# Kernel optimization log

Measured on AMD Instinct MI355X. Metric: run time of the kernel, lower is better.

## Reference

```python
import jax, jax.numpy as jnp
import numpy as np

B, L, D, V, d, N, H = 16, 1024, 50, 129, 64, 2, 8
DK = d // H           # 8
DFF = 2 * d           # 128
CVE = int(np.sqrt(d)) # 8
EPS = 1e-07 ** 2      # module squares epsilon
MASK_ATTN = -1e-30    # Transformer mask_value (as in source)
MASK_POOL = -1e+30    # Attention-pooling mask_value


def setup_inputs() -> dict:
    key = jax.random.key(0)
    ks = jax.random.split(key, 32)
    g = lambda i, shape, s=0.02: (jax.random.normal(ks[i], shape, dtype=jnp.float32) * s)
    inp = {
        'demo':   jax.random.normal(ks[0], (B, D), dtype=jnp.float32),
        'times':  jax.random.uniform(ks[1], (B, L), dtype=jnp.float32),
        'values': jax.random.normal(ks[2], (B, L), dtype=jnp.float32),
        'varis':  jax.random.randint(ks[3], (B, L), 0, V + 1),
        # variable embedding table
        'emb': g(4, (V + 1, d), 0.05),
        # CVE for values: Linear(1,CVE)+tanh+Linear(CVE,d,no bias)
        'vW1': g(5, (1, CVE), 0.5), 'vb1': jnp.zeros((CVE,), jnp.float32), 'vW2': g(6, (CVE, d), 0.1),
        # CVE for times
        'tW1': g(7, (1, CVE), 0.5), 'tb1': jnp.zeros((CVE,), jnp.float32), 'tW2': g(8, (CVE, d), 0.1),
        # Transformer params
        'Wq': g(9,  (N, H, d, DK), 0.1), 'Wk': g(10, (N, H, d, DK), 0.1),
        'Wv': g(11, (N, H, d, DK), 0.1), 'Wo': g(12, (N, H * DK, d), 0.1),
        'W1': g(13, (N, d, DFF), 0.1), 'b1': jnp.zeros((N, DFF), jnp.float32),
        'W2': g(14, (N, DFF, d), 0.1), 'b2': jnp.zeros((N, d), jnp.float32),
        'gamma': jnp.ones((2 * N,), jnp.float32), 'beta': jnp.zeros((2 * N,), jnp.float32),
        # Attention pooling: Linear(d,2d)+tanh+Linear(2d,1,no bias)
        'aW1': g(15, (d, 2 * d), 0.1), 'ab1': jnp.zeros((2 * d,), jnp.float32), 'aW2': g(16, (2 * d, 1), 0.1),
        # demo stack: Linear(D,2d)+tanh+Linear(2d,d)+tanh
        'dW1': g(17, (D, 2 * d), 0.1), 'db1': jnp.zeros((2 * d,), jnp.float32),
        'dW2': g(18, (2 * d, d), 0.1), 'db2': jnp.zeros((d,), jnp.float32),
        # output head: Linear(2d,1)+sigmoid+flatten
        'Wout': g(19, (2 * d, 1), 0.1), 'bout': jnp.zeros((1,), jnp.float32),
    }
    return inp


def _ln(X, g, b):
    mean = jnp.mean(X, axis=-1, keepdims=True)
    var = jnp.mean(jnp.square(X - mean), axis=-1, keepdims=True)
    return (X - mean) / jnp.sqrt(var + EPS) * g + b


def _forward(demo, times, values, varis, emb, vW1, vb1, vW2, tW1, tb1, tW2,
             Wq, Wk, Wv, Wo, W1, b1, W2, b2, gamma, beta,
             aW1, ab1, aW2, dW1, db1, dW2, db2, Wout, bout):
    mask = (varis > 0).astype(jnp.float32)  # [B,L]
    demo_enc = jnp.tanh(jnp.tanh(demo @ dW1 + db1) @ dW2 + db2)  # [B,d]
    varis_emb = emb[varis]                                       # [B,L,d]
    values_emb = jnp.tanh(values[..., None] @ vW1 + vb1) @ vW2   # [B,L,d]
    times_emb = jnp.tanh(times[..., None] @ tW1 + tb1) @ tW2     # [B,L,d]
    X = varis_emb + values_emb + times_emb

    mb = mask[:, None, None, :]  # [B,1,1,L] broadcasts over heads & query rows
    for i in range(N):
        q = jnp.einsum('bld,hdk->bhlk', X, Wq[i])
        k = jnp.einsum('bld,hdk->bhlk', X, Wk[i])
        v = jnp.einsum('bld,hdk->bhlk', X, Wv[i])
        A = jnp.einsum('bhlk,bhmk->bhlm', q, k)      # no 1/sqrt(dk) scaling (faithful)
        A = mb * A + (1.0 - mb) * MASK_ATTN
        A = jax.nn.softmax(A, axis=-1)
        O = jnp.einsum('bhlm,bhmk->bhlk', A, v)      # [B,H,L,DK]
        conc = jnp.transpose(O, (0, 2, 1, 3)).reshape(O.shape[0], O.shape[2], H * DK)
        X = X + conc @ Wo[i]
        X = _ln(X, gamma[2 * i], beta[2 * i])
        ffn = jax.nn.relu(X @ W1[i] + b1[i]) @ W2[i] + b2[i]
        X = X + ffn
        X = _ln(X, gamma[2 * i + 1], beta[2 * i + 1])

    aw = jnp.tanh(X @ aW1 + ab1) @ aW2               # [B,L,1]
    m = mask[..., None]
    aw = jax.nn.softmax(m * aw + (1.0 - m) * MASK_POOL, axis=-2)
    fused = jnp.sum(X * aw, axis=-2)                 # [B,d]
    conc = jnp.concatenate([fused, demo_enc], axis=-1)
    return jax.nn.sigmoid(conc @ Wout + bout).reshape(-1)  # [B]


def reference(demo, times, values, varis, emb, vW1, vb1, vW2, tW1, tb1, tW2,
              Wq, Wk, Wv, Wo, W1, b1, W2, b2, gamma, beta,
              aW1, ab1, aW2, dW1, db1, dW2, db2, Wout, bout):
    return _forward(demo, times, values, varis, emb, vW1, vb1, vW2, tW1, tb1, tW2,
                    Wq, Wk, Wv, Wo, W1, b1, W2, b2, gamma, beta,
                    aW1, ab1, aW2, dW1, db1, dW2, db2, Wout, bout)
```

## Files before the change

### kernel.cpp

```cpp
#include <hip/hip_runtime.h>
#include <math.h>


typedef __bf16 bf16x8 __attribute__((ext_vector_type(8)));
typedef __bf16 bf16x2 __attribute__((ext_vector_type(2)));
typedef float f32x16 __attribute__((ext_vector_type(16)));
typedef unsigned int uint4e __attribute__((ext_vector_type(4)));
typedef unsigned long long u64;

static __device__ __forceinline__ float wave_sum64(float x) {
#pragma unroll
    for (int off = 32; off > 0; off >>= 1) x += __shfl_xor(x, off, 64);
    return x;
}

static __device__ __forceinline__ unsigned pack2(float a, float b) {
    bf16x2 t; t[0] = (__bf16)a; t[1] = (__bf16)b;
    return __builtin_bit_cast(unsigned, t);
}

static __device__ __forceinline__ float exp2fast(float x) {
#if defined(__has_builtin) && __has_builtin(__builtin_amdgcn_exp2f)
    return __builtin_amdgcn_exp2f(x);
#else
    return exp2f(x);
#endif
}

static __device__ __forceinline__ void plswap(unsigned v, unsigned& lo, unsigned& hi_) {
#if defined(__has_builtin) && __has_builtin(__builtin_amdgcn_permlane32_swap)
    auto r = __builtin_amdgcn_permlane32_swap(v, v, false, false);
    lo = r[0]; hi_ = r[1];
#else
    unsigned x = __shfl_xor(v, 32, 64);
    bool h = (threadIdx.x & 32) != 0;
    lo = h ? x : v;
    hi_ = h ? v : x;
#endif
}

__global__ __launch_bounds__(256) void embed_kernel(
    const float* __restrict__ times, const float* __restrict__ values,
    const int* __restrict__ varis, const float* __restrict__ emb,
    const float* __restrict__ vW1, const float* __restrict__ vb1, const float* __restrict__ vW2,
    const float* __restrict__ tW1, const float* __restrict__ tb1, const float* __restrict__ tW2,
    float* __restrict__ X, float* __restrict__ mask)
{
    int row = blockIdx.x * 4 + (threadIdx.x >> 6);
    int c   = threadIdx.x & 63;
    float v = values[row];
    float t = times[row];
    int var = varis[row];
    if (c == 0) mask[row] = (var > 0) ? 1.0f : 0.0f;
    float th = 0.f;
    if (c < 8)       th = tanhf(fmaf(v, vW1[c], vb1[c]));
    else if (c < 16) th = tanhf(fmaf(t, tW1[c - 8], tb1[c - 8]));
    float acc = emb[var * 64 + c];
#pragma unroll
    for (int j = 0; j < 8; ++j) {
        acc = fmaf(__shfl(th, j, 64),     vW2[j * 64 + c], acc);
        acc = fmaf(__shfl(th, j + 8, 64), tW2[j * 64 + c], acc);
    }
    X[row * 64 + c] = acc;
}

__global__ __launch_bounds__(128) void demo_kernel(
    const float* __restrict__ demo, const float* __restrict__ dW1, const float* __restrict__ db1,
    const float* __restrict__ dW2, const float* __restrict__ db2, float* __restrict__ denc)
{
    __shared__ float sh[128];
    int b = blockIdx.x;
    int t = threadIdx.x;
    float a = db1[t];
    for (int j = 0; j < 50; ++j) a = fmaf(demo[b * 50 + j], dW1[j * 128 + t], a);
    sh[t] = tanhf(a);
    __syncthreads();
    if (t < 64) {
        float a2 = db2[t];
#pragma unroll 8
        for (int j = 0; j < 128; ++j) a2 = fmaf(sh[j], dW2[j * 64 + t], a2);
        denc[b * 64 + t] = tanhf(a2);
    }
}

__global__ __launch_bounds__(256) void qkv_kernel(
    const float* __restrict__ X, const float* __restrict__ mask,
    const float* __restrict__ Wq, const float* __restrict__ Wk, const float* __restrict__ Wv,
    __bf16* __restrict__ qbf, __bf16* __restrict__ kbf, __bf16* __restrict__ vtb)
{
    __shared__ __align__(16) unsigned char qsm[52224];
    float* sWq = (float*)qsm;
    float* sWk = sWq + 4352;
    float* sWv = sWk + 4352;
    int tid = threadIdx.x;
    for (int idx = tid; idx < 4096; idx += 256) {
        int h = idx >> 9, c = (idx >> 3) & 63, kk = idx & 7;
        int o = h * 8 + kk;
        sWq[o * 68 + c] = Wq[idx];
        sWk[o * 68 + c] = Wk[idx];
        sWv[o * 68 + c] = Wv[idx];
    }
    int row0 = blockIdx.x * 16;
    __syncthreads();
    int lane = tid & 63;
    int wv4 = (tid >> 6) * 4;
    float aq[4] = {0.f, 0.f, 0.f, 0.f};
    float ak[4] = {0.f, 0.f, 0.f, 0.f};
    float av[4] = {0.f, 0.f, 0.f, 0.f};
#pragma unroll
    for (int c = 0; c < 64; c += 4) {
        float4 xv[4];
#pragma unroll
        for (int rr = 0; rr < 4; ++rr)
            xv[rr] = *(const float4*)(X + (row0 + wv4 + rr) * 64 + c);
        float4 wq = *(const float4*)(sWq + lane * 68 + c);
        float4 wk = *(const float4*)(sWk + lane * 68 + c);
        float4 wvv= *(const float4*)(sWv + lane * 68 + c);
#pragma unroll
        for (int rr = 0; rr < 4; ++rr) {
            aq[rr] = fmaf(xv[rr].x, wq.x, aq[rr]);  aq[rr] = fmaf(xv[rr].y, wq.y, aq[rr]);
            aq[rr] = fmaf(xv[rr].z, wq.z, aq[rr]);  aq[rr] = fmaf(xv[rr].w, wq.w, aq[rr]);
            ak[rr] = fmaf(xv[rr].x, wk.x, ak[rr]);  ak[rr] = fmaf(xv[rr].y, wk.y, ak[rr]);
            ak[rr] = fmaf(xv[rr].z, wk.z, ak[rr]);  ak[rr] = fmaf(xv[rr].w, wk.w, ak[rr]);
            av[rr] = fmaf(xv[rr].x, wvv.x, av[rr]); av[rr] = fmaf(xv[rr].y, wvv.y, av[rr]);
            av[rr] = fmaf(xv[rr].z, wvv.z, av[rr]); av[rr] = fmaf(xv[rr].w, wvv.w, av[rr]);
        }
    }
    float aqr[4], akr[4], avr[4];
#pragma unroll
    for (int rr = 0; rr < 4; ++rr) {
        float km = mask[row0 + wv4 + rr];
        aqr[rr] = aq[rr] * 1.4426950408889634f;
        akr[rr] = (km != 0.f) ? ak[rr] : 0.f;
        avr[rr] = av[rr];
    }
    __syncthreads();
    __bf16* sQb = (__bf16*)qsm;
    __bf16* sKb = (__bf16*)(qsm + 2304);
    __bf16* sVt = (__bf16*)(qsm + 4608);
    int h = lane >> 3, kk = lane & 7;
#pragma unroll
    for (int rr = 0; rr < 4; ++rr) {
        int r = wv4 + rr;
        sQb[h * 136 + r * 8 + kk] = (__bf16)aqr[rr];
        sKb[h * 136 + r * 8 + kk] = (__bf16)akr[rr];
        sVt[lane * 18 + r] = (__bf16)avr[rr];
    }
    __syncthreads();
    int b = row0 >> 10, l0 = row0 & 1023;
    unsigned* qg = (unsigned*)qbf;
    unsigned* kg = (unsigned*)kbf;
    const unsigned* q32 = (const unsigned*)sQb;
    const unsigned* k32 = (const unsigned*)sKb;
#pragma unroll
    for (int it = 0; it < 2; ++it) {
        int idx = it * 256 + tid;
        int hh = idx >> 6, w = idx & 63;
        int gbase = ((b * 8 + hh) * 1024 + l0) * 4;
        qg[gbase + w] = q32[hh * 68 + w];
        kg[gbase + w] = k32[hh * 68 + w];
    }
#pragma unroll
    for (int it = 0; it < 2; ++it) {
        int idx = it * 256 + tid;
        int hkk = idx >> 3, lp = idx & 7;
        unsigned w = ((const unsigned*)sVt)[hkk * 9 + lp];
        int hh = hkk >> 3, k2 = hkk & 7;
        ((unsigned*)(vtb + (b * 8 + hh) * 8192 + k2 * 1024 + l0))[lp] = w;
    }
}

__global__ __launch_bounds__(256, 2) void attn_mfma_kernel(
    const __bf16* __restrict__ qbf, const __bf16* __restrict__ kbf,
    const __bf16* __restrict__ vtb, float* __restrict__ Opart, float* __restrict__ ssum)
{
    __shared__ __align__(16) unsigned char smem[17600];
    __bf16* sK  = (__bf16*)smem;
    __bf16* sVT = (__bf16*)(smem + 8192);

    int tid   = threadIdx.x;
    int bh    = blockIdx.x & 127;
    int chunk = (blockIdx.x >> 7) & 7;
    int s     = blockIdx.x >> 10;

    const u64* kg = (const u64*)(kbf + bh * 8192 + s * 4096);
    u64* sKq = (u64*)sK;
#pragma unroll
    for (int i = 0; i < 4; ++i) sKq[i * 256 + tid] = kg[i * 256 + tid];

    const u64* vgb = (const u64*)(vtb + bh * 8192 + s * 512);
#pragma unroll
    for (int it = 0; it < 4; ++it) {
        int idx = it * 256 + tid;
        int r = idx >> 7, w = idx & 127;
        ((u64*)(sVT + r * 520))[w] = vgb[r * 256 + w];
    }
    ((unsigned*)(sVT + 8 * 520))[tid] = 0x3f803f80u;
    __syncthreads();

    int lane = tid & 63;
    int wv   = tid >> 6;
    int hi   = lane >> 5;
    int l31  = lane & 31;
    unsigned hm = hi ? 0u : 0xffffffffu;

    int qrow = chunk * 128 + wv * 32 + l31;

    bf16x8 qf;
    {
        const __bf16* qp = qbf + (bh * 1024 + qrow) * 8;
        uint4e qa = *(const uint4e*)qp;
        qa[0] &= hm; qa[1] &= hm; qa[2] &= hm; qa[3] &= hm;
        qf = __builtin_bit_cast(bf16x8, qa);
    }

    f32x16 acc, zc;
#pragma unroll
    for (int i = 0; i < 16; ++i) { acc[i] = 0.f; zc[i] = 0.f; }

    const bf16x8* sKv = (const bf16x8*)sK;
    const __bf16* vbase = sVT + (l31 < 8 ? l31 : 8) * 520;

#pragma unroll 2
    for (int kt = 0; kt < 16; ++kt) {
        bf16x8 kf = sKv[kt * 32 + l31];
        f32x16 st = __builtin_amdgcn_mfma_f32_32x32x16_bf16(kf, qf, zc, 0, 0, 0);
        float p[16];
#pragma unroll
        for (int r = 0; r < 16; ++r) p[r] = exp2fast(st[r]);

#pragma unroll
        for (int h = 0; h < 2; ++h) {
            unsigned La0, Ha0, Lb0, Hb0, La1, Ha1, Lb1, Hb1;
            int g0 = 2 * h, g1 = 2 * h + 1;
            plswap(pack2(p[4 * g0 + 0], p[4 * g0 + 1]), La0, Ha0);
            plswap(pack2(p[4 * g0 + 2], p[4 * g0 + 3]), Lb0, Hb0);
            plswap(pack2(p[4 * g1 + 0], p[4 * g1 + 1]), La1, Ha1);
            plswap(pack2(p[4 * g1 + 2], p[4 * g1 + 3]), Lb1, Hb1);
            uint4e pw;
            pw[0] = hi ? La1 : La0;
            pw[1] = hi ? Lb1 : Lb0;
            pw[2] = hi ? Ha1 : Ha0;
            pw[3] = hi ? Hb1 : Hb0;
            bf16x8 vf = *(const bf16x8*)(vbase + kt * 32 + 16 * h + 8 * hi);
            acc = __builtin_amdgcn_mfma_f32_32x32x16_bf16(vf, __builtin_bit_cast(bf16x8, pw), acc, 0, 0, 0);
        }
    }

    __syncthreads();
    float* sO = (float*)smem;
    int qloc = wv * 32 + l31;
    float4 t0;
    t0.x = acc[0]; t0.y = acc[1]; t0.z = acc[2]; t0.w = acc[3];
    *(float4*)(sO + qloc * 12 + 4 * hi) = t0;
    __syncthreads();
    float* og = Opart + ((s * 128 + bh) * 1024 + chunk * 128) * 8;
    {
        int q = tid >> 1, part = tid & 1;
        *(float4*)(og + tid * 4) = *(const float4*)(sO + q * 12 + part * 4);
    }
    if (!hi) {
        ssum[(s * 128 + bh) * 1024 + qrow] = acc[4];
    }
}

__global__ __launch_bounds__(256) void proj_ln_kernel(
    float* __restrict__ X, const float* __restrict__ Opart, const float* __restrict__ ssum,
    const float* __restrict__ Wo, const float* __restrict__ gamma, const float* __restrict__ beta,
    int gi)
{
    __shared__ float sWo[4096];
    __shared__ float so[16][64];
    int tid = threadIdx.x;
    for (int idx = tid; idx < 4096; idx += 256) sWo[idx] = Wo[idx];
    int row0 = blockIdx.x * 16;
#pragma unroll
    for (int it = 0; it < 4; ++it) {
        int idx = it * 256 + tid;
        int r = idx >> 6, j = idx & 63;
        int grow = row0 + r;
        int b = grow >> 10, l = grow & 1023;
        int bh = b * 8 + (j >> 3);
        int base = (bh * 1024 + l) * 8 + (j & 7);
        float num = Opart[base] + Opart[1048576 + base];
        int sb = bh * 1024 + l;
        float den = ssum[sb] + ssum[131072 + sb];
        so[r][j] = num / den;
    }
    __syncthreads();
    int lane = tid & 63, wv = tid >> 6;
#pragma unroll
    for (int it = 0; it < 4; ++it) {
        int r = it * 4 + wv;
        float acc = 0.f;
#pragma unroll 8
        for (int j = 0; j < 64; ++j) acc = fmaf(so[r][j], sWo[j * 64 + lane], acc);
        float x = X[(row0 + r) * 64 + lane] + acc;
        float mean = wave_sum64(x) * (1.0f / 64.0f);
        float dx = x - mean;
        float var = wave_sum64(dx * dx) * (1.0f / 64.0f);
        X[(row0 + r) * 64 + lane] = dx * rsqrtf(var + 1e-14f) * gamma[gi] + beta[gi];
    }
}

__global__ __launch_bounds__(256) void ffn1_kernel(
    const float* __restrict__ X, const float* __restrict__ W1, const float* __restrict__ b1,
    float* __restrict__ hid)
{
    __shared__ __align__(16) float sW[128 * 68];
    __shared__ __align__(16) float sX[2048];
    int tid = threadIdx.x;
    for (int idx = tid; idx < 8192; idx += 256) {
        int c = idx >> 7, j = idx & 127;
        sW[j * 68 + c] = W1[idx];
    }
    int row0 = blockIdx.x * 32;
    for (int i = tid; i < 512; i += 256)
        ((float4*)sX)[i] = ((const float4*)(X + row0 * 64))[i];
    __syncthreads();
    int j4 = tid & 31;
    int r0 = (tid >> 5) * 4;
    float acc[4][4];
#pragma unroll
    for (int jj = 0; jj < 4; ++jj) {
        float bb = b1[j4 + 32 * jj];
#pragma unroll
        for (int rr = 0; rr < 4; ++rr) acc[rr][jj] = bb;
    }
#pragma unroll 2
    for (int c = 0; c < 64; c += 4) {
        float4 xv[4];
#pragma unroll
        for (int rr = 0; rr < 4; ++rr) xv[rr] = *(const float4*)(sX + (r0 + rr) * 64 + c);
#pragma unroll
        for (int jj = 0; jj < 4; ++jj) {
            float4 wv = *(const float4*)(sW + (j4 + 32 * jj) * 68 + c);
#pragma unroll
            for (int rr = 0; rr < 4; ++rr) {
                acc[rr][jj] = fmaf(xv[rr].x, wv.x, acc[rr][jj]);
                acc[rr][jj] = fmaf(xv[rr].y, wv.y, acc[rr][jj]);
                acc[rr][jj] = fmaf(xv[rr].z, wv.z, acc[rr][jj]);
                acc[rr][jj] = fmaf(xv[rr].w, wv.w, acc[rr][jj]);
            }
        }
    }
#pragma unroll
    for (int rr = 0; rr < 4; ++rr)
#pragma unroll
        for (int jj = 0; jj < 4; ++jj)
            hid[(row0 + r0 + rr) * 128 + j4 + 32 * jj] = fmaxf(acc[rr][jj], 0.0f);
}

__global__ __launch_bounds__(256) void ffn2_ln_kernel(
    float* __restrict__ X, const float* __restrict__ hid,
    const float* __restrict__ W2, const float* __restrict__ b2,
    const float* __restrict__ gamma, const float* __restrict__ beta, int gi)
{
    __shared__ __align__(16) float sW[64 * 132];
    __shared__ __align__(16) float sO[2048];
    int tid = threadIdx.x;
    for (int idx = tid; idx < 8192; idx += 256) {
        int j = idx >> 6, c = idx & 63;
        sW[c * 132 + j] = W2[idx];
    }
    int row0 = blockIdx.x * 32;
    __syncthreads();
    int c4 = tid & 15;
    int r0 = (tid >> 4) * 2;
    float acc[2][4];
#pragma unroll
    for (int cc = 0; cc < 4; ++cc) {
        float bb = b2[c4 + 16 * cc];
        acc[0][cc] = bb; acc[1][cc] = bb;
    }
#pragma unroll 2
    for (int jc = 0; jc < 128; jc += 4) {
        float4 hv[2];
#pragma unroll
        for (int rr = 0; rr < 2; ++rr)
            hv[rr] = *(const float4*)(hid + (row0 + r0 + rr) * 128 + jc);
#pragma unroll
        for (int cc = 0; cc < 4; ++cc) {
            float4 wvv = *(const float4*)(sW + (c4 + 16 * cc) * 132 + jc);
#pragma unroll
            for (int rr = 0; rr < 2; ++rr) {
                acc[rr][cc] = fmaf(hv[rr].x, wvv.x, acc[rr][cc]);
                acc[rr][cc] = fmaf(hv[rr].y, wvv.y, acc[rr][cc]);
                acc[rr][cc] = fmaf(hv[rr].z, wvv.z, acc[rr][cc]);
                acc[rr][cc] = fmaf(hv[rr].w, wvv.w, acc[rr][cc]);
            }
        }
    }
#pragma unroll
    for (int rr = 0; rr < 2; ++rr)
#pragma unroll
        for (int cc = 0; cc < 4; ++cc)
            sO[(r0 + rr) * 64 + c4 + 16 * cc] = acc[rr][cc];
    __syncthreads();
    int lane = tid & 63, wv = tid >> 6;
#pragma unroll
    for (int it = 0; it < 8; ++it) {
        int r = wv * 8 + it;
        float x = X[(row0 + r) * 64 + lane] + sO[r * 64 + lane];
        float mean = wave_sum64(x) * (1.0f / 64.0f);
        float dx = x - mean;
        float var = wave_sum64(dx * dx) * (1.0f / 64.0f);
        X[(row0 + r) * 64 + lane] = dx * rsqrtf(var + 1e-14f) * gamma[gi] + beta[gi];
    }
}

__global__ __launch_bounds__(256) void aw_kernel(
    const float* __restrict__ X, const float* __restrict__ aW1, const float* __restrict__ ab1,
    const float* __restrict__ aW2, float* __restrict__ aw)
{
    __shared__ __align__(16) float sW[128 * 68];
    __shared__ __align__(16) float sX[2048];
    int tid = threadIdx.x;
    for (int idx = tid; idx < 8192; idx += 256) {
        int c = idx >> 7, j = idx & 127;
        sW[j * 68 + c] = aW1[idx];
    }
    int row0 = blockIdx.x * 32;
    for (int i = tid; i < 512; i += 256)
        ((float4*)sX)[i] = ((const float4*)(X + row0 * 64))[i];
    __syncthreads();
    int j4 = tid & 31;
    int r0 = (tid >> 5) * 4;
    float acc[4][4];
#pragma unroll
    for (int jj = 0; jj < 4; ++jj) {
        float bb = ab1[j4 + 32 * jj];
#pragma unroll
        for (int rr = 0; rr < 4; ++rr) acc[rr][jj] = bb;
    }
#pragma unroll 2
    for (int c = 0; c < 64; c += 4) {
        float4 xv[4];
#pragma unroll
        for (int rr = 0; rr < 4; ++rr) xv[rr] = *(const float4*)(sX + (r0 + rr) * 64 + c);
#pragma unroll
        for (int jj = 0; jj < 4; ++jj) {
            float4 wv = *(const float4*)(sW + (j4 + 32 * jj) * 68 + c);
#pragma unroll
            for (int rr = 0; rr < 4; ++rr) {
                acc[rr][jj] = fmaf(xv[rr].x, wv.x, acc[rr][jj]);
                acc[rr][jj] = fmaf(xv[rr].y, wv.y, acc[rr][jj]);
                acc[rr][jj] = fmaf(xv[rr].z, wv.z, acc[rr][jj]);
                acc[rr][jj] = fmaf(xv[rr].w, wv.w, acc[rr][jj]);
            }
        }
    }
    float a2[4];
#pragma unroll
    for (int jj = 0; jj < 4; ++jj) a2[jj] = aW2[j4 + 32 * jj];
    int lane = tid & 63;
#pragma unroll
    for (int rr = 0; rr < 4; ++rr) {
        float part = tanhf(acc[rr][0]) * a2[0] + tanhf(acc[rr][1]) * a2[1]
                   + tanhf(acc[rr][2]) * a2[2] + tanhf(acc[rr][3]) * a2[3];
#pragma unroll
        for (int off = 16; off > 0; off >>= 1) part += __shfl_xor(part, off, 64);
        if ((lane & 31) == 0) aw[row0 + r0 + rr] = part;
    }
}

__global__ __launch_bounds__(1024) void pool_kernel(
    const float* __restrict__ X, const float* __restrict__ aw, const float* __restrict__ mask,
    const float* __restrict__ denc, const float* __restrict__ Wout,
    const float* __restrict__ bout, float* __restrict__ out)
{
    __shared__ float sp[1024];
    __shared__ float red[16];
    __shared__ float red2[16];
    __shared__ float sf[16][64];
    int b = blockIdx.x, tid = threadIdx.x;
    float s = (mask[b * 1024 + tid] != 0.0f) ? aw[b * 1024 + tid] : -1e30f;
    float m = s;
#pragma unroll
    for (int off = 32; off > 0; off >>= 1) m = fmaxf(m, __shfl_xor(m, off, 64));
    if ((tid & 63) == 0) red[tid >> 6] = m;
    __syncthreads();
    float gmax = red[0];
#pragma unroll
    for (int i = 1; i < 16; ++i) gmax = fmaxf(gmax, red[i]);
    float p = __expf(s - gmax);
    sp[tid] = p;
    float psum = wave_sum64(p);
    if ((tid & 63) == 0) red2[tid >> 6] = psum;
    __syncthreads();
    float tot = 0.f;
#pragma unroll
    for (int i = 0; i < 16; ++i) tot += red2[i];
    float inv = 1.0f / tot;
    int c = tid & 63, g = tid >> 6;
    int l0 = g * 64;
    float f = 0.f;
#pragma unroll 4
    for (int i = 0; i < 64; ++i)
        f = fmaf(sp[l0 + i], X[(b * 1024 + l0 + i) * 64 + c], f);
    sf[g][c] = f;
    __syncthreads();
    if (tid < 64) {
        float fc = 0.f;
#pragma unroll
        for (int ch = 0; ch < 16; ++ch) fc += sf[ch][tid];
        fc *= inv;
        float contrib = fc * Wout[tid] + denc[b * 64 + tid] * Wout[64 + tid];
        contrib = wave_sum64(contrib);
        if (tid == 0) out[b] = 1.0f / (1.0f + __expf(-(contrib + bout[0])));
    }
}

extern "C" void kernel_launch(void* const* d_in, const int* in_sizes, int n_in,
                              void* d_out, int out_size, void* d_ws, size_t ws_size,
                              hipStream_t stream)
{
    const float* demo  = (const float*)d_in[0];
    const float* times = (const float*)d_in[1];
    const float* values= (const float*)d_in[2];
    const int*   varis = (const int*)d_in[3];
    const float* emb   = (const float*)d_in[4];
    const float* vW1   = (const float*)d_in[5];
    const float* vb1   = (const float*)d_in[6];
    const float* vW2   = (const float*)d_in[7];
    const float* tW1   = (const float*)d_in[8];
    const float* tb1   = (const float*)d_in[9];
    const float* tW2   = (const float*)d_in[10];
    const float* Wq    = (const float*)d_in[11];
    const float* Wk    = (const float*)d_in[12];
    const float* Wv    = (const float*)d_in[13];
    const float* Wo    = (const float*)d_in[14];
    const float* W1    = (const float*)d_in[15];
    const float* b1    = (const float*)d_in[16];
    const float* W2    = (const float*)d_in[17];
    const float* b2    = (const float*)d_in[18];
    const float* gamma = (const float*)d_in[19];
    const float* beta  = (const float*)d_in[20];
    const float* aW1   = (const float*)d_in[21];
    const float* ab1   = (const float*)d_in[22];
    const float* aW2   = (const float*)d_in[23];
    const float* dW1   = (const float*)d_in[24];
    const float* db1   = (const float*)d_in[25];
    const float* dW2   = (const float*)d_in[26];
    const float* db2   = (const float*)d_in[27];
    const float* Wout  = (const float*)d_in[28];
    const float* bout  = (const float*)d_in[29];
    float* out = (float*)d_out;

    float* ws     = (float*)d_ws;
    float* X      = ws;
    float* mask   = X + 1048576;
    __bf16* qbf   = (__bf16*)(mask + 16384);
    __bf16* kbf   = qbf + 1048576;
    __bf16* vtb   = kbf + 1048576;
    float* Opart  = (float*)(vtb + 1048576);
    float* ssum   = Opart + 2097152;
    float* awb    = ssum + 262144;
    float* denc   = awb + 16384;
    float* hid    = denc + 1024;

    embed_kernel<<<4096, 256, 0, stream>>>(times, values, varis, emb, vW1, vb1, vW2, tW1, tb1, tW2, X, mask);
    demo_kernel<<<16, 128, 0, stream>>>(demo, dW1, db1, dW2, db2, denc);
    for (int i = 0; i < 2; ++i) {
        qkv_kernel<<<1024, 256, 0, stream>>>(X, mask, Wq + i * 4096, Wk + i * 4096, Wv + i * 4096,
                                             qbf, kbf, vtb);
        attn_mfma_kernel<<<2048, 256, 0, stream>>>(qbf, kbf, vtb, Opart, ssum);
        proj_ln_kernel<<<1024, 256, 0, stream>>>(X, Opart, ssum, Wo + i * 4096, gamma, beta, 2 * i);
        ffn1_kernel<<<512, 256, 0, stream>>>(X, W1 + i * 8192, b1 + i * 128, hid);
        ffn2_ln_kernel<<<512, 256, 0, stream>>>(X, hid, W2 + i * 8192, b2 + i * 64,
                                                gamma, beta, 2 * i + 1);
    }
    aw_kernel<<<512, 256, 0, stream>>>(X, aW1, ab1, aW2, awb);
    pool_kernel<<<16, 1024, 0, stream>>>(X, awb, mask, denc, Wout, bout, out);
}
```

Before: 189.4 us.

## Drop split-K in attention, process full key range per block and normalize in-kernel

The attention kernel no longer splits the 1024 keys across two blocks with partial outputs and partial softmax sums. Each block now loads all keys and values into shared memory, loops over 32 key tiles, and divides by the row sum before writing the final output. The K fragment for the next tile is prefetched one iteration ahead. This removes the partial-sum buffers and the combine/division work in proj_ln, but halves the grid to 1024 blocks and doubles shared memory per block, which may reduce occupancy and parallelism.

```diff
diff --git a/kernel.cpp b/kernel.cpp
--- a/kernel.cpp
+++ b/kernel.cpp
@@ -172,30 +172,33 @@
 
 __global__ __launch_bounds__(256, 2) void attn_mfma_kernel(
     const __bf16* __restrict__ qbf, const __bf16* __restrict__ kbf,
-    const __bf16* __restrict__ vtb, float* __restrict__ Opart, float* __restrict__ ssum)
-{
-    __shared__ __align__(16) unsigned char smem[17600];
+    const __bf16* __restrict__ vtb, float* __restrict__ O)
+{
+    __shared__ __align__(16) unsigned char smem[35008];
     __bf16* sK  = (__bf16*)smem;
-    __bf16* sVT = (__bf16*)(smem + 8192);
+    __bf16* sVT = (__bf16*)(smem + 16384);
 
     int tid   = threadIdx.x;
     int bh    = blockIdx.x & 127;
-    int chunk = (blockIdx.x >> 7) & 7;
-    int s     = blockIdx.x >> 10;
-
-    const u64* kg = (const u64*)(kbf + bh * 8192 + s * 4096);
+    int chunk = blockIdx.x >> 7;
+
+    const u64* kg = (const u64*)(kbf + bh * 8192);
     u64* sKq = (u64*)sK;
 #pragma unroll
-    for (int i = 0; i < 4; ++i) sKq[i * 256 + tid] = kg[i * 256 + tid];
-
-    const u64* vgb = (const u64*)(vtb + bh * 8192 + s * 512);
-#pragma unroll
-    for (int it = 0; it < 4; ++it) {
+    for (int i = 0; i < 8; ++i) sKq[i * 256 + tid] = kg[i * 256 + tid];
+
+    const u64* vgb = (const u64*)(vtb + bh * 8192);
+#pragma unroll
+    for (int it = 0; it < 8; ++it) {
         int idx = it * 256 + tid;
-        int r = idx >> 7, w = idx & 127;
-        ((u64*)(sVT + r * 520))[w] = vgb[r * 256 + w];
-    }
-    ((unsigned*)(sVT + 8 * 520))[tid] = 0x3f803f80u;
+        int r = idx >> 8, w = idx & 255;
+        ((u64*)(sVT + r * 1032))[w] = vgb[idx];
+    }
+    {
+        unsigned* p1 = (unsigned*)(sVT + 8 * 1032);
+        p1[tid] = 0x3f803f80u;
+        p1[256 + tid] = 0x3f803f80u;
+    }
     __syncthreads();
 
     int lane = tid & 63;
@@ -219,11 +222,12 @@
     for (int i = 0; i < 16; ++i) { acc[i] = 0.f; zc[i] = 0.f; }
 
     const bf16x8* sKv = (const bf16x8*)sK;
-    const __bf16* vbase = sVT + (l31 < 8 ? l31 : 8) * 520;
-
+    const __bf16* vbase = sVT + (l31 < 8 ? l31 : 8) * 1032;
+
+    bf16x8 kf = sKv[l31];
 #pragma unroll 2
-    for (int kt = 0; kt < 16; ++kt) {
-        bf16x8 kf = sKv[kt * 32 + l31];
+    for (int kt = 0; kt < 32; ++kt) {
+        bf16x8 kfn = sKv[((kt + 1) & 31) * 32 + l31];
         f32x16 st = __builtin_amdgcn_mfma_f32_32x32x16_bf16(kf, qf, zc, 0, 0, 0);
         float p[16];
 #pragma unroll
@@ -245,27 +249,26 @@
             bf16x8 vf = *(const bf16x8*)(vbase + kt * 32 + 16 * h + 8 * hi);
             acc = __builtin_amdgcn_mfma_f32_32x32x16_bf16(vf, __builtin_bit_cast(bf16x8, pw), acc, 0, 0, 0);
         }
-    }
-
+        kf = kfn;
+    }
+
+    float inv = 1.0f / acc[4];
     __syncthreads();
     float* sO = (float*)smem;
     int qloc = wv * 32 + l31;
     float4 t0;
-    t0.x = acc[0]; t0.y = acc[1]; t0.z = acc[2]; t0.w = acc[3];
+    t0.x = acc[0] * inv; t0.y = acc[1] * inv; t0.z = acc[2] * inv; t0.w = acc[3] * inv;
     *(float4*)(sO + qloc * 12 + 4 * hi) = t0;
     __syncthreads();
-    float* og = Opart + ((s * 128 + bh) * 1024 + chunk * 128) * 8;
+    float* og = O + (bh * 1024 + chunk * 128) * 8;
     {
         int q = tid >> 1, part = tid & 1;
         *(float4*)(og + tid * 4) = *(const float4*)(sO + q * 12 + part * 4);
     }
-    if (!hi) {
-        ssum[(s * 128 + bh) * 1024 + qrow] = acc[4];
-    }
 }
 
 __global__ __launch_bounds__(256) void proj_ln_kernel(
-    float* __restrict__ X, const float* __restrict__ Opart, const float* __restrict__ ssum,
+    float* __restrict__ X, const float* __restrict__ O,
     const float* __restrict__ Wo, const float* __restrict__ gamma, const float* __restrict__ beta,
     int gi)
 {
@@ -281,11 +284,7 @@
         int grow = row0 + r;
         int b = grow >> 10, l = grow & 1023;
         int bh = b * 8 + (j >> 3);
-        int base = (bh * 1024 + l) * 8 + (j & 7);
-        float num = Opart[base] + Opart[1048576 + base];
-        int sb = bh * 1024 + l;
-        float den = ssum[sb] + ssum[131072 + sb];
-        so[r][j] = num / den;
+        so[r][j] = O[(bh * 1024 + l) * 8 + (j & 7)];
     }
     __syncthreads();
     int lane = tid & 63, wv = tid >> 6;
@@ -553,9 +552,8 @@
     __bf16* qbf   = (__bf16*)(mask + 16384);
     __bf16* kbf   = qbf + 1048576;
     __bf16* vtb   = kbf + 1048576;
-    float* Opart  = (float*)(vtb + 1048576);
-    float* ssum   = Opart + 2097152;
-    float* awb    = ssum + 262144;
+    float* Ob     = (float*)(vtb + 1048576);
+    float* awb    = Ob + 1048576;
     float* denc   = awb + 16384;
     float* hid    = denc + 1024;
 
@@ -564,8 +562,8 @@
     for (int i = 0; i < 2; ++i) {
         qkv_kernel<<<1024, 256, 0, stream>>>(X, mask, Wq + i * 4096, Wk + i * 4096, Wv + i * 4096,
                                              qbf, kbf, vtb);
-        attn_mfma_kernel<<<2048, 256, 0, stream>>>(qbf, kbf, vtb, Opart, ssum);
-        proj_ln_kernel<<<1024, 256, 0, stream>>>(X, Opart, ssum, Wo + i * 4096, gamma, beta, 2 * i);
+        attn_mfma_kernel<<<1024, 256, 0, stream>>>(qbf, kbf, vtb, Ob);
+        proj_ln_kernel<<<1024, 256, 0, stream>>>(X, Ob, Wo + i * 4096, gamma, beta, 2 * i);
         ffn1_kernel<<<512, 256, 0, stream>>>(X, W1 + i * 8192, b1 + i * 128, hid);
         ffn2_ln_kernel<<<512, 256, 0, stream>>>(X, hid, W2 + i * 8192, b2 + i * 64,
                                                 gamma, beta, 2 * i + 1);
```

Measured after the change: 185.5 us. -2.1%, faster.
